# Kernel optimization log

Measured on AMD Instinct MI355X. Metric: run time of the kernel, lower is better.

Reference implementation:

```python
import jax, jax.numpy as jnp
import numpy as np

N_NODES = 100000
N_EDGES = 300000
D = 128
HID = 128

def setup_inputs() -> dict:
    key = jax.random.key(0)
    ks = jax.random.split(key, 12)
    s = lambda fan_in: 1.0 / np.sqrt(fan_in)
    return {
        "user_emb": jax.random.normal(ks[0], (N_NODES, D), jnp.float32),
        "item_emb": jax.random.normal(ks[1], (N_NODES, D), jnp.float32),
        "ei_ui": jax.random.randint(ks[2], (2, N_EDGES), 0, N_NODES, jnp.int64),
        "ei_iu": jax.random.randint(ks[3], (2, N_EDGES), 0, N_NODES, jnp.int64),
        "W_bi_ui": jax.random.normal(ks[4], (2 * D, HID), jnp.float32) * s(2 * D),
        "b_bi_ui": jnp.zeros((HID,), jnp.float32),
        "W1_ui": jax.random.normal(ks[5], (HID, HID), jnp.float32) * s(HID),
        "b1_ui": jnp.zeros((HID,), jnp.float32),
        "W2_ui": jax.random.normal(ks[6], (HID, 1), jnp.float32) * s(HID),
        "b2_ui": jnp.zeros((1,), jnp.float32),
        "W_bi_iu": jax.random.normal(ks[7], (2 * D, HID), jnp.float32) * s(2 * D),
        "b_bi_iu": jnp.zeros((HID,), jnp.float32),
        "W1_iu": jax.random.normal(ks[8], (HID, HID), jnp.float32) * s(HID),
        "b1_iu": jnp.zeros((HID,), jnp.float32),
        "W2_iu": jax.random.normal(ks[9], (HID, 1), jnp.float32) * s(HID),
        "b2_iu": jnp.zeros((1,), jnp.float32),
    }

def _decode_edge_type(src_emb, dst_emb, edge_index, W_bi, b_bi, W1, b1, W2, b2):
    # gather endpoint embeddings and concat -> [E, 2D]
    e = jnp.concatenate([src_emb[edge_index[0]], dst_emb[edge_index[1]]], axis=1)
    h = jax.nn.elu(e @ W_bi + b_bi)          # bilinear -> ELU
    h = jax.nn.elu(h @ W1 + b1)              # linear1 -> ELU
    p = jax.nn.sigmoid(h @ W2 + b2)          # linear2 -> sigmoid
    return p.reshape(-1)                     # [E]

def reference(user_emb, item_emb, ei_ui, ei_iu,
              W_bi_ui, b_bi_ui, W1_ui, b1_ui, W2_ui, b2_ui,
              W_bi_iu, b_bi_iu, W1_iu, b1_iu, W2_iu, b2_iu):
    # edge type (user, clicks, item): source=user, target=item
    p_ui = _decode_edge_type(user_emb, item_emb, ei_ui,
                             W_bi_ui, b_bi_ui, W1_ui, b1_ui, W2_ui, b2_ui)
    # edge type (item, clicked_by, user): source=item, target=user
    p_iu = _decode_edge_type(item_emb, user_emb, ei_iu,
                             W_bi_iu, b_bi_iu, W1_iu, b1_iu, W2_iu, b2_iu)
    return jnp.stack([p_ui, p_iu])  # [2, E]
```

## Files before the change

kernel.cpp:

```cpp
#include <hip/hip_runtime.h>

typedef __attribute__((ext_vector_type(8))) short short8;
typedef __attribute__((ext_vector_type(4))) float float4v;
typedef __attribute__((ext_vector_type(4))) int int4v;

#define E_EDGES 300000
#define EPB 128
#define NBLK ((E_EDGES + EPB - 1) / EPB)
#define TAB_ELEMS 12800000

__device__ __forceinline__ short f2bf(float f) {
    unsigned u = __float_as_uint(f);
    return (short)((u + 0x7FFFu + ((u >> 16) & 1u)) >> 16);
}
__device__ __forceinline__ unsigned pk_bf16(float a, float b) {
    unsigned ua = __float_as_uint(a), ub = __float_as_uint(b);
    ua += 0x7FFFu + ((ua >> 16) & 1u);
    ub += 0x7FFFu + ((ub >> 16) & 1u);
    return __builtin_amdgcn_perm(ub, ua, 0x07060302);
}
__device__ __forceinline__ void cp16(const void* g, void* l) {
    __builtin_amdgcn_global_load_lds(
        (const __attribute__((address_space(1))) unsigned int*)g,
        (__attribute__((address_space(3))) unsigned int*)l, 16, 0, 0);
}

__global__ void prep_all(const float* __restrict__ ue, const float* __restrict__ ie,
                         const float* __restrict__ Wbi_ui, const float* __restrict__ W1_ui,
                         const float* __restrict__ Wbi_iu, const float* __restrict__ W1_iu,
                         short* __restrict__ ws) {
    __shared__ short tr[64 * 68];
    const int t = blockIdx.y;
    const int tid = threadIdx.x;
    if (blockIdx.x < 1024) {
        const float* src = t ? ie : ue;
        short* dst = ws + 98304 + (size_t)t * TAB_ELEMS;
        const int stride = 1024 * 256;
        for (int g = blockIdx.x * 256 + tid; g < TAB_ELEMS / 8; g += stride) {
            const float* p = src + (size_t)g * 8;
            float4v v0 = ((const float4v*)p)[0];
            float4v v1 = ((const float4v*)p)[1];
            int4v w = { (int)pk_bf16(v0[0], v0[1]), (int)pk_bf16(v0[2], v0[3]),
                        (int)pk_bf16(v1[0], v1[1]), (int)pk_bf16(v1[2], v1[3]) };
            *(int4v*)(dst + (size_t)g * 8) = w;
        }
        return;
    }
    const int m = blockIdx.x - 1024;
    const float* W; int k0, n0, obase;
    if (m < 8) {
        int kt = m >> 1, nh = m & 1;
        W = t ? Wbi_iu : Wbi_ui; k0 = kt * 64; n0 = nh * 64;
        obase = t * 32768 + kt * 8192;
    } else {
        int mm = m - 8; int kt = mm >> 1, nh = mm & 1;
        W = t ? W1_iu : W1_ui; k0 = kt * 64; n0 = nh * 64;
        obase = 65536 + t * 16384 + kt * 8192;
    }
    for (int it = 0; it < 16; ++it) {
        int flat = it * 256 + tid;
        int kk = flat >> 6, nn = flat & 63;
        tr[nn * 68 + kk] = f2bf(W[(size_t)(k0 + kk) * 128 + n0 + nn]);
    }
    __syncthreads();
    for (int it = 0; it < 16; ++it) {
        int flat = it * 256 + tid;
        int nn = flat >> 6, kk = flat & 63;
        int n = n0 + nn;
        ws[obase + n * 64 + (kk ^ ((n & 7) << 3))] = tr[nn * 68 + kk];
    }
}

template<bool BF16G>
__launch_bounds__(256, 3)
__global__ void edge_decoder(
    const float* __restrict__ user_emb, const float* __restrict__ item_emb,
    const int* __restrict__ ei_ui, const int* __restrict__ ei_iu,
    const float* __restrict__ b_bi_ui, const float* __restrict__ b1_ui,
    const float* __restrict__ W2_ui, const float* __restrict__ b2_ui,
    const float* __restrict__ b_bi_iu, const float* __restrict__ b1_iu,
    const float* __restrict__ W2_iu, const float* __restrict__ b2_iu,
    const short* __restrict__ ws, const short* __restrict__ tab,
    float* __restrict__ out)
{
    __shared__ short Blds[128 * 64];
    __shared__ short Hlds[4 * 32 * 136];

    const int type = blockIdx.y;
    const int e0 = blockIdx.x * EPB;
    const int tid = threadIdx.x;
    const int wave = tid >> 6, lane = tid & 63;
    const int q = lane >> 4, ln = lane & 15;

    const int*   ei   = type ? ei_iu : ei_ui;
    const float* bbi  = type ? b_bi_iu : b_bi_ui;
    const float* b1v  = type ? b1_iu : b1_ui;
    const float* W2v  = type ? W2_iu : W2_ui;
    const float* b2v  = type ? b2_iu : b2_ui;
    const short* WbiT = ws + type * 32768;
    const short* W1T  = ws + 65536 + type * 16384;

    int si[2], di[2];
    for (int mt = 0; mt < 2; ++mt) {
        int erow = e0 + wave * 32 + mt * 16 + ln;
        int safe = (erow < E_EDGES) ? erow : 0;
        si[mt] = ei[safe];
        di[mt] = ei[E_EDGES + safe];
    }

    for (int c = 0; c < 4; ++c)
        cp16(WbiT + c * 2048 + tid * 8, Blds + c * 2048 + tid * 8);

    short8 a[2][8];
    if (BF16G) {
        for (int mt = 0; mt < 2; ++mt) {
            const short* sp = tab + (size_t)(type ? TAB_ELEMS : 0) + (size_t)si[mt] * 128;
            const short* dp = tab + (size_t)(type ? 0 : TAB_ELEMS) + (size_t)di[mt] * 128;
            for (int ks = 0; ks < 4; ++ks)
                a[mt][ks] = *(const short8*)(sp + ks * 32 + q * 8);
            for (int ks = 4; ks < 8; ++ks)
                a[mt][ks] = *(const short8*)(dp + (ks - 4) * 32 + q * 8);
        }
    } else {
        const float* srcT = type ? item_emb : user_emb;
        const float* dstT = type ? user_emb : item_emb;
        for (int mt = 0; mt < 2; ++mt)
            for (int ks = 0; ks < 8; ++ks) {
                const float* p = (ks < 4) ? (srcT + (size_t)si[mt] * 128 + ks * 32 + q * 8)
                                          : (dstT + (size_t)di[mt] * 128 + (ks - 4) * 32 + q * 8);
                float4v v0 = ((const float4v*)p)[0];
                float4v v1 = ((const float4v*)p)[1];
                int4v w = { (int)pk_bf16(v0[0], v0[1]), (int)pk_bf16(v0[2], v0[3]),
                            (int)pk_bf16(v1[0], v1[1]), (int)pk_bf16(v1[2], v1[3]) };
                a[mt][ks] = *(short8*)&w;
            }
    }

    float4v acc[2][8];
    for (int nt = 0; nt < 8; ++nt) {
        float bb = bbi[nt * 16 + ln];
        acc[0][nt] = (float4v){bb, bb, bb, bb};
        acc[1][nt] = acc[0][nt];
    }

    const int swz = (ln & 7) << 3;

    for (int kt = 0; kt < 4; ++kt) {
        __syncthreads();
        for (int ks2 = 0; ks2 < 2; ++ks2) {
            int ka = (ks2 * 32 + q * 8) ^ swz;
            int ks = kt * 2 + ks2;
            for (int nt = 0; nt < 8; ++nt) {
                short8 bf = *(const short8*)&Blds[(nt * 16 + ln) * 64 + ka];
                acc[0][nt] = __builtin_amdgcn_mfma_f32_16x16x32_bf16(a[0][ks], bf, acc[0][nt], 0, 0, 0);
                acc[1][nt] = __builtin_amdgcn_mfma_f32_16x16x32_bf16(a[1][ks], bf, acc[1][nt], 0, 0, 0);
            }
        }
        __syncthreads();
        const short* nxt = (kt < 3) ? (WbiT + (kt + 1) * 8192) : W1T;
        for (int c = 0; c < 4; ++c)
            cp16(nxt + c * 2048 + tid * 8, Blds + c * 2048 + tid * 8);
    }

    short* Hw = Hlds + wave * (32 * 136);
    for (int mt = 0; mt < 2; ++mt)
        for (int nt = 0; nt < 8; ++nt) {
            int col = nt * 16 + ln;
            float4v v = acc[mt][nt];
            for (int r = 0; r < 4; ++r) {
                float x = v[r];
                float h = x > 0.f ? x : (__expf(x) - 1.f);
                Hw[(mt * 16 + q * 4 + r) * 136 + col] = f2bf(h);
            }
        }
    short8 a2[2][4];
    for (int mt = 0; mt < 2; ++mt)
        for (int ks = 0; ks < 4; ++ks)
            a2[mt][ks] = *(const short8*)&Hw[(mt * 16 + ln) * 136 + ks * 32 + q * 8];

    for (int nt = 0; nt < 8; ++nt) {
        float bb = b1v[nt * 16 + ln];
        acc[0][nt] = (float4v){bb, bb, bb, bb};
        acc[1][nt] = acc[0][nt];
    }

    for (int kt = 0; kt < 2; ++kt) {
        __syncthreads();
        for (int ks2 = 0; ks2 < 2; ++ks2) {
            int ka = (ks2 * 32 + q * 8) ^ swz;
            int ks = kt * 2 + ks2;
            for (int nt = 0; nt < 8; ++nt) {
                short8 bf = *(const short8*)&Blds[(nt * 16 + ln) * 64 + ka];
                acc[0][nt] = __builtin_amdgcn_mfma_f32_16x16x32_bf16(a2[0][ks], bf, acc[0][nt], 0, 0, 0);
                acc[1][nt] = __builtin_amdgcn_mfma_f32_16x16x32_bf16(a2[1][ks], bf, acc[1][nt], 0, 0, 0);
            }
        }
        __syncthreads();
        if (kt == 0)
            for (int c = 0; c < 4; ++c)
                cp16(W1T + 8192 + c * 2048 + tid * 8, Blds + c * 2048 + tid * 8);
    }

    for (int mt = 0; mt < 2; ++mt) {
        float s0 = 0.f, s1 = 0.f, s2 = 0.f, s3 = 0.f;
        for (int nt = 0; nt < 8; ++nt) {
            float wv = W2v[nt * 16 + ln];
            float4v v = acc[mt][nt];
            float x;
            x = v[0]; x = x > 0.f ? x : (__expf(x) - 1.f); s0 += x * wv;
            x = v[1]; x = x > 0.f ? x : (__expf(x) - 1.f); s1 += x * wv;
            x = v[2]; x = x > 0.f ? x : (__expf(x) - 1.f); s2 += x * wv;
            x = v[3]; x = x > 0.f ? x : (__expf(x) - 1.f); s3 += x * wv;
        }
        for (int off = 1; off < 16; off <<= 1) {
            s0 += __shfl_xor(s0, off);
            s1 += __shfl_xor(s1, off);
            s2 += __shfl_xor(s2, off);
            s3 += __shfl_xor(s3, off);
        }
        if (ln < 4) {
            float sv = (ln == 0) ? s0 : (ln == 1) ? s1 : (ln == 2) ? s2 : s3;
            int e = e0 + wave * 32 + mt * 16 + q * 4 + ln;
            if (e < E_EDGES) {
                float z = sv + b2v[0];
                out[type * E_EDGES + e] = 1.f / (1.f + __expf(-z));
            }
        }
    }
}

extern "C" void kernel_launch(void* const* d_in, const int* in_sizes, int n_in,
                              void* d_out, int out_size, void* d_ws, size_t ws_size,
                              hipStream_t stream) {
    const float* user_emb = (const float*)d_in[0];
    const float* item_emb = (const float*)d_in[1];
    const int*   ei_ui    = (const int*)d_in[2];
    const int*   ei_iu    = (const int*)d_in[3];
    const float* W_bi_ui  = (const float*)d_in[4];
    const float* b_bi_ui  = (const float*)d_in[5];
    const float* W1_ui    = (const float*)d_in[6];
    const float* b1_ui    = (const float*)d_in[7];
    const float* W2_ui    = (const float*)d_in[8];
    const float* b2_ui    = (const float*)d_in[9];
    const float* W_bi_iu  = (const float*)d_in[10];
    const float* b_bi_iu  = (const float*)d_in[11];
    const float* W1_iu    = (const float*)d_in[12];
    const float* b1_iu    = (const float*)d_in[13];
    const float* W2_iu    = (const float*)d_in[14];
    const float* b2_iu    = (const float*)d_in[15];
    short* ws  = (short*)d_ws;
    short* tab = ws + 98304;
    float* out = (float*)d_out;

    const size_t need = 98304u * 2u + (size_t)2 * TAB_ELEMS * 2u;

    if (ws_size >= need) {
        hipLaunchKernelGGL(prep_all, dim3(1036, 2), dim3(256), 0, stream,
                           user_emb, item_emb, W_bi_ui, W1_ui, W_bi_iu, W1_iu, ws);
        edge_decoder<true><<<dim3(NBLK, 2), dim3(256), 0, stream>>>(
            user_emb, item_emb, ei_ui, ei_iu,
            b_bi_ui, b1_ui, W2_ui, b2_ui,
            b_bi_iu, b1_iu, W2_iu, b2_iu,
            ws, tab, out);
    } else {
        hipLaunchKernelGGL(prep_all, dim3(1036, 2), dim3(256), 0, stream,
                           user_emb, item_emb, W_bi_ui, W1_ui, W_bi_iu, W1_iu, ws);
        edge_decoder<false><<<dim3(NBLK, 2), dim3(256), 0, stream>>>(
            user_emb, item_emb, ei_ui, ei_iu,
            b_bi_ui, b1_ui, W2_ui, b2_ui,
            b_bi_iu, b1_iu, W2_iu, b2_iu,
            ws, tab, out);
    }
}
```

Baseline: 253.5 us.

## Double-buffer weight tiles in LDS and reuse buffer for hidden activations

Replaces the single weight LDS tile and separate per-wave hidden buffer with two ping-pong weight buffers. Each weight chunk is prefetched into the alternate buffer while MFMAs run on the current one, halving the barriers per k-step. The hidden activations are staged in the idle buffer with an XOR swizzle, which shrinks LDS use enough to raise the occupancy target from 3 to 4 blocks. MFMA sections get raised wave priority. The tighter occupancy bound may cap registers and cause spills, and the buffer reuse relies on correct barrier placement.

```diff
diff --git a/kernel.cpp b/kernel.cpp
--- a/kernel.cpp
+++ b/kernel.cpp
@@ -72,7 +72,7 @@
 }
 
 template<bool BF16G>
-__launch_bounds__(256, 3)
+__launch_bounds__(256, 4)
 __global__ void edge_decoder(
     const float* __restrict__ user_emb, const float* __restrict__ item_emb,
     const int* __restrict__ ei_ui, const int* __restrict__ ei_iu,
@@ -83,8 +83,7 @@
     const short* __restrict__ ws, const short* __restrict__ tab,
     float* __restrict__ out)
 {
-    __shared__ short Blds[128 * 64];
-    __shared__ short Hlds[4 * 32 * 136];
+    __shared__ short Blds[2][128 * 64];
 
     const int type = blockIdx.y;
     const int e0 = blockIdx.x * EPB;
@@ -100,6 +99,9 @@
     const short* WbiT = ws + type * 32768;
     const short* W1T  = ws + 65536 + type * 16384;
 
+    for (int c = 0; c < 4; ++c)
+        cp16(WbiT + c * 2048 + tid * 8, &Blds[0][c * 2048 + tid * 8]);
+
     int si[2], di[2];
     for (int mt = 0; mt < 2; ++mt) {
         int erow = e0 + wave * 32 + mt * 16 + ln;
@@ -107,9 +109,6 @@
         si[mt] = ei[safe];
         di[mt] = ei[E_EDGES + safe];
     }
-
-    for (int c = 0; c < 4; ++c)
-        cp16(WbiT + c * 2048 + tid * 8, Blds + c * 2048 + tid * 8);
 
     short8 a[2][8];
     if (BF16G) {
@@ -145,38 +144,44 @@
 
     const int swz = (ln & 7) << 3;
 
+    int cur = 0;
     for (int kt = 0; kt < 4; ++kt) {
         __syncthreads();
+        const short* nxt = (kt < 3) ? (WbiT + (kt + 1) * 8192) : W1T;
+        for (int c = 0; c < 4; ++c)
+            cp16(nxt + c * 2048 + tid * 8, &Blds[cur ^ 1][c * 2048 + tid * 8]);
+        __builtin_amdgcn_s_setprio(1);
         for (int ks2 = 0; ks2 < 2; ++ks2) {
             int ka = (ks2 * 32 + q * 8) ^ swz;
             int ks = kt * 2 + ks2;
             for (int nt = 0; nt < 8; ++nt) {
-                short8 bf = *(const short8*)&Blds[(nt * 16 + ln) * 64 + ka];
+                short8 bf = *(const short8*)&Blds[cur][(nt * 16 + ln) * 64 + ka];
                 acc[0][nt] = __builtin_amdgcn_mfma_f32_16x16x32_bf16(a[0][ks], bf, acc[0][nt], 0, 0, 0);
                 acc[1][nt] = __builtin_amdgcn_mfma_f32_16x16x32_bf16(a[1][ks], bf, acc[1][nt], 0, 0, 0);
             }
         }
-        __syncthreads();
-        const short* nxt = (kt < 3) ? (WbiT + (kt + 1) * 8192) : W1T;
-        for (int c = 0; c < 4; ++c)
-            cp16(nxt + c * 2048 + tid * 8, Blds + c * 2048 + tid * 8);
-    }
-
-    short* Hw = Hlds + wave * (32 * 136);
-    for (int mt = 0; mt < 2; ++mt)
+        __builtin_amdgcn_s_setprio(0);
+        cur ^= 1;
+    }
+
+    __syncthreads();
+
+    short* Hw = &Blds[cur ^ 1][wave * 2048];
+    short8 a2[2][4];
+    for (int mt = 0; mt < 2; ++mt) {
         for (int nt = 0; nt < 8; ++nt) {
-            int col = nt * 16 + ln;
             float4v v = acc[mt][nt];
             for (int r = 0; r < 4; ++r) {
                 float x = v[r];
                 float h = x > 0.f ? x : (__expf(x) - 1.f);
-                Hw[(mt * 16 + q * 4 + r) * 136 + col] = f2bf(h);
-            }
-        }
-    short8 a2[2][4];
-    for (int mt = 0; mt < 2; ++mt)
+                int row = q * 4 + r;
+                int g = (nt * 2 + (ln >> 3)) ^ (row & 7);
+                Hw[row * 128 + g * 8 + (ln & 7)] = f2bf(h);
+            }
+        }
         for (int ks = 0; ks < 4; ++ks)
-            a2[mt][ks] = *(const short8*)&Hw[(mt * 16 + ln) * 136 + ks * 32 + q * 8];
+            a2[mt][ks] = *(const short8*)&Hw[ln * 128 + (((ks * 4 + q) ^ (ln & 7)) << 3)];
+    }
 
     for (int nt = 0; nt < 8; ++nt) {
         float bb = b1v[nt * 16 + ln];
@@ -184,21 +189,24 @@
         acc[1][nt] = acc[0][nt];
     }
 
+    __syncthreads();
+    for (int c = 0; c < 4; ++c)
+        cp16(W1T + 8192 + c * 2048 + tid * 8, &Blds[cur ^ 1][c * 2048 + tid * 8]);
+
     for (int kt = 0; kt < 2; ++kt) {
-        __syncthreads();
+        if (kt == 1) __syncthreads();
+        __builtin_amdgcn_s_setprio(1);
         for (int ks2 = 0; ks2 < 2; ++ks2) {
             int ka = (ks2 * 32 + q * 8) ^ swz;
             int ks = kt * 2 + ks2;
             for (int nt = 0; nt < 8; ++nt) {
-                short8 bf = *(const short8*)&Blds[(nt * 16 + ln) * 64 + ka];
+                short8 bf = *(const short8*)&Blds[cur][(nt * 16 + ln) * 64 + ka];
                 acc[0][nt] = __builtin_amdgcn_mfma_f32_16x16x32_bf16(a2[0][ks], bf, acc[0][nt], 0, 0, 0);
                 acc[1][nt] = __builtin_amdgcn_mfma_f32_16x16x32_bf16(a2[1][ks], bf, acc[1][nt], 0, 0, 0);
             }
         }
-        __syncthreads();
-        if (kt == 0)
-            for (int c = 0; c < 4; ++c)
-                cp16(W1T + 8192 + c * 2048 + tid * 8, Blds + c * 2048 + tid * 8);
+        __builtin_amdgcn_s_setprio(0);
+        cur ^= 1;
     }
 
     for (int mt = 0; mt < 2; ++mt) {
```

After: 261.1 us. +3.0%, slower.
